# Kernel optimization log

Hardware: AMD Instinct MI355X
Metric: run time of the kernel (lower is better)

The kernel has to match this reference:

```python
import jax, jax.numpy as jnp
import numpy as np

THRESH = 0.001
RADIUS = 0.1
NSAMPLE = 8
FRAME_DIM = 6
LOSS_WEIGHT = 1.0
EPS = 1e-7


def _ball_query(new_xyz, xyz, radius, nsample):
    # new_xyz: [N,3] query points; xyz: [F,3] candidate points
    # pointnet2 semantics: first `nsample` in-radius indices (in order),
    # remaining slots filled with the first found index (0 if none).
    d2 = jnp.sum((new_xyz[:, None, :] - xyz[None, :, :]) ** 2, axis=-1)  # [N,F]
    mask = d2 < radius * radius
    order = jnp.argsort(~mask, axis=1)[:, :nsample]          # stable: in-radius idx first
    cnt = jnp.sum(mask, axis=1)                               # [N]
    valid = jnp.arange(nsample)[None, :] < cnt[:, None]       # [N,nsample]
    return jnp.where(valid, order, order[:, :1])              # [N,nsample] int


def _face_normals(verts, faces):
    # verts: [M,3], faces: [F,3] -> unit normals [F,3]
    v = verts[faces]                                           # [F,3,3]
    n = jnp.cross(v[:, 1] - v[:, 0], v[:, 2] - v[:, 0])        # [F,3]
    norm = jnp.linalg.norm(n, axis=-1, keepdims=True)
    return n / jnp.maximum(norm, EPS)


def _contact_error_single(pred, state, h_state, h_faces):
    x_t1 = pred[:, :3]                                         # [N,3]
    x_t0 = state[:, :3]                                        # [N,3]
    h_t1 = h_state[:, :3]                                      # [M,3]
    h_t0 = h_state[:, FRAME_DIM:FRAME_DIM + 3]                 # [M,3]
    h_face_pos = jnp.mean(h_t1[h_faces], axis=-2)              # [F,3]
    h_face_prev_pos = jnp.mean(h_t0[h_faces], axis=-2)         # [F,3]
    h_face_normal = _face_normals(h_t1, h_faces)               # [F,3]
    idx = _ball_query(x_t0, h_face_prev_pos, RADIUS, NSAMPLE)  # [N,S]
    grouped_pos = h_face_pos[idx]                              # [N,S,3]
    grouped_normal = h_face_normal[idx]                        # [N,S,3]
    xyz_diff = jnp.sum((x_t1[:, None, :] - grouped_pos) * grouped_normal,
                       axis=-1, keepdims=True)                 # [N,S,1]
    interpen = jnp.maximum(THRESH - xyz_diff, 0.0)
    loss = jnp.sum(interpen ** 3, axis=-2)                     # [N,1]
    return jnp.mean(loss)                                      # reduction='mean'


def setup_inputs() -> dict:
    key = jax.random.key(0)
    k1, k2, k3, k4 = jax.random.split(key, 4)
    B, N, M, F = 2, 20000, 6890, 13776
    pred = jax.random.normal(k1, (B, N, 3), dtype=jnp.float32)
    state = jax.random.normal(k2, (B, N, 3), dtype=jnp.float32)
    h_state = jax.random.normal(k3, (B, M, 9), dtype=jnp.float32)
    h_faces = jax.random.randint(k4, (B, F, 3), 0, M, dtype=jnp.int32)
    return {"pred": pred, "state": state, "h_state": h_state, "h_faces": h_faces}


def reference(pred, state, h_state, h_faces):
    per_sample = jax.vmap(_contact_error_single)(pred, state, h_state, h_faces)  # [B]
    return jnp.mean(per_sample) * LOSS_WEIGHT
```

## Files before the change

kernel.cpp:

```cpp
#include <hip/hip_runtime.h>
#include <limits.h>

#define NB      2
#define N_Q     20000
#define NBQ     (NB * N_Q)
#define M_V     6890
#define N_F     13776
#define NBF     (NB * N_F)
#define RAD2    0.01f
#define THRESH  0.001f
#define EPSN    1e-7f
#define SCALE   (1.0f / (float)(NB * N_Q))

#define GDIM    12
#define NCELLS  (GDIM * GDIM * GDIM)
#define T_CELLS (NB * NCELLS)
#define H_INV   5.0f
#define ORG     (-1.2f)

#define CAP     128

#define QPB     8
#define QBLOCKS (NBQ / QPB)

__device__ __forceinline__ int cell_coord(float x) {
    int g = (int)floorf((x - ORG) * H_INV);
    return min(max(g, 0), GDIM - 1);
}

__device__ __forceinline__ void axis_window(float v, int& lo, int& hi) {
    float s  = (v - ORG) * H_INV;
    float fl = floorf(s);
    int g_u  = (int)fl;
    int g    = min(max(g_u, 0), GDIM - 1);
    int sy   = ((s - fl) >= 0.5f) ? 1 : -1;
    int g2   = min(max(g_u + sy, 0), GDIM - 1);
    lo = min(g, g2);
    hi = max(g, g2);
}

__device__ __forceinline__ float wave_add_f(float v) {
    #pragma unroll
    for (int m = 32; m; m >>= 1) v += __shfl_xor(v, m);
    return v;
}
__device__ __forceinline__ int half_min_i(int v) {
    #pragma unroll
    for (int m = 16; m; m >>= 1) v = min(v, __shfl_xor(v, m));
    return v;
}

__global__ __launch_bounds__(256) void face_kernel(
    const float* __restrict__ h_state,
    const int*   __restrict__ h_faces,
    float4* __restrict__ posn,
    float4* __restrict__ buckets,
    int* __restrict__ cellCnt)
{
    int t = blockIdx.x * 256 + threadIdx.x;
    if (t >= NBF) return;
    int b = t / N_F;
    const int* fc = h_faces + (size_t)t * 3;
    int i0 = fc[0], i1 = fc[1], i2 = fc[2];
    const float* hs = h_state + (size_t)b * M_V * 9;

    const float* v0 = hs + (size_t)i0 * 9;
    const float* v1 = hs + (size_t)i1 * 9;
    const float* v2 = hs + (size_t)i2 * 9;

    float ax = v0[0], ay = v0[1], az = v0[2];
    float bx = v1[0], by = v1[1], bz = v1[2];
    float cx = v2[0], cy = v2[1], cz = v2[2];

    float px = (ax + bx + cx) / 3.0f;
    float py = (ay + by + cy) / 3.0f;
    float pz = (az + bz + cz) / 3.0f;

    float e1x = bx - ax, e1y = by - ay, e1z = bz - az;
    float e2x = cx - ax, e2y = cy - ay, e2z = cz - az;
    float nx = e1y * e2z - e1z * e2y;
    float ny = e1z * e2x - e1x * e2z;
    float nz = e1x * e2y - e1y * e2x;
    float nrm = sqrtf(nx * nx + ny * ny + nz * nz);
    float den = fmaxf(nrm, EPSN);
    nx /= den; ny /= den; nz /= den;

    float qx = (v0[6] + v1[6] + v2[6]) / 3.0f;
    float qy = (v0[7] + v1[7] + v2[7]) / 3.0f;
    float qz = (v0[8] + v1[8] + v2[8]) / 3.0f;

    posn[2 * t]     = make_float4(px, py, pz, 0.0f);
    posn[2 * t + 1] = make_float4(nx, ny, nz, 0.0f);

    int gx = cell_coord(qx), gy = cell_coord(qy), gz = cell_coord(qz);
    int cid = b * NCELLS + (gz * GDIM + gy) * GDIM + gx;
    int slot = atomicAdd(&cellCnt[cid], 1);
    if (slot < CAP)
        buckets[(size_t)cid * CAP + slot] = make_float4(qx, qy, qz, __int_as_float(t));
}

#define CSW(a, b) { int _mn = min(a, b); int _mx = max(a, b); a = _mn; b = _mx; }

__global__ __launch_bounds__(256) void query_kernel(
    const float*  __restrict__ state,
    const float*  __restrict__ pred,
    const float4* __restrict__ buckets,
    const float4* __restrict__ posn,
    const int* __restrict__ cellCnt,
    float* __restrict__ partials)
{
    __shared__ float ws[QPB];

    int tid  = threadIdx.x;
    int l32  = tid & 31;
    int hw   = tid >> 5;
    int q    = blockIdx.x * QPB + hw;
    int b    = (q >= N_Q) ? 1 : 0;

    const float* st = state + (size_t)q * 3;
    float qx = st[0], qy = st[1], qz = st[2];
    const float* pr = pred + (size_t)q * 3;
    float x = pr[0], y = pr[1], z = pr[2];

    float4 P0 = posn[2 * (b * N_F)];
    float4 N0 = posn[2 * (b * N_F) + 1];

    int xlo, xhi, ylo, yhi, zlo, zhi;
    axis_window(qx, xlo, xhi);
    axis_window(qy, ylo, yhi);
    axis_window(qz, zlo, zhi);

    int cum1, cum2, cum3, cum4, cum5, cum6, cum7, cum8;
    int off0, off1, off2, off3, off4, off5, off6, off7;
    {
        int bN = b * NCELLS;
        #define CELL(CI, CUMP, CUMN, OFFR)                                  \
        {                                                                   \
            int gz = zlo + ((CI) >> 2);                                     \
            int gy = ylo + (((CI) >> 1) & 1);                               \
            int gx = xlo + ((CI) & 1);                                      \
            int len = 0, base = 0;                                          \
            if (gz <= zhi && gy <= yhi && gx <= xhi) {                      \
                int c = bN + (gz * GDIM + gy) * GDIM + gx;                  \
                len = cellCnt[c];                                           \
                base = c * CAP;                                             \
            }                                                               \
            OFFR = base - CUMP;                                             \
            CUMN = CUMP + len;                                              \
        }
        int c0 = 0;
        CELL(0, c0,   cum1, off0)
        CELL(1, cum1, cum2, off1)
        CELL(2, cum2, cum3, off2)
        CELL(3, cum3, cum4, off3)
        CELL(4, cum4, cum5, off4)
        CELL(5, cum5, cum6, off5)
        CELL(6, cum6, cum7, off6)
        CELL(7, cum7, cum8, off7)
        #undef CELL
    }
    int C = cum8;

    int s0 = INT_MAX, s1 = INT_MAX, s2 = INT_MAX, s3 = INT_MAX;
    int s4 = INT_MAX, s5 = INT_MAX, s6 = INT_MAX, s7 = INT_MAX;
    int cnt = 0;
    float fsum = 0.0f;
    int   lmin = INT_MAX;
    float fmin = 0.0f;

    int iters = (C + 31) >> 5;
    for (int it = 0; it < iters; ++it) {
        int k = (it << 5) + l32;
        int addr = off0 + k;
        addr = (k >= cum1) ? off1 + k : addr;
        addr = (k >= cum2) ? off2 + k : addr;
        addr = (k >= cum3) ? off3 + k : addr;
        addr = (k >= cum4) ? off4 + k : addr;
        addr = (k >= cum5) ? off5 + k : addr;
        addr = (k >= cum6) ? off6 + k : addr;
        addr = (k >= cum7) ? off7 + k : addr;
        if (k < C) {
            float4 p = buckets[addr];
            float ddx = p.x - qx, ddy = p.y - qy, ddz = p.z - qz;
            float d2 = ddx * ddx + ddy * ddy + ddz * ddz;
            if (d2 < RAD2) {
                ++cnt;
                int tf = __float_as_int(p.w);
                float4 P  = posn[2 * tf];
                float4 Nn = posn[2 * tf + 1];
                float d = (x - P.x) * Nn.x + (y - P.y) * Nn.y + (z - P.z) * Nn.z;
                float ip = fmaxf(THRESH - d, 0.0f);
                float f = ip * ip * ip;
                fsum += f;
                if (tf < lmin) { lmin = tf; fmin = f; }
                if (tf < s7) {
                    s7 = tf;
                    CSW(s6, s7); CSW(s5, s6); CSW(s4, s5); CSW(s3, s4);
                    CSW(s2, s3); CSW(s1, s2); CSW(s0, s1);
                }
            }
        }
    }

    int   c_ = cnt;
    float fs = fsum;
    int   lm = lmin;
    float fm = fmin;
    #pragma unroll
    for (int m = 16; m; m >>= 1) {
        int   oc = __shfl_xor(c_, m);
        float os = __shfl_xor(fs, m);
        int   ol = __shfl_xor(lm, m);
        float of = __shfl_xor(fm, m);
        c_ += oc;
        fs += os;
        if (ol < lm) { lm = ol; fm = of; }
    }
    int cnt_tot = c_;

    float lsum;
    if (cnt_tot == 0) {
        float d0 = (x - P0.x) * N0.x + (y - P0.y) * N0.y + (z - P0.z) * N0.z;
        float ip0 = fmaxf(THRESH - d0, 0.0f);
        lsum = 8.0f * (ip0 * ip0 * ip0);
    } else if (cnt_tot <= 8) {
        lsum = fs + (float)(8 - cnt_tot) * fm;
    } else {
        int t0, t1, t2, t3, t4, t5, t6, t7;
#define EXTRACT(TK)                                                      \
        {                                                                \
            int m = half_min_i(s0);                                      \
            TK = m;                                                      \
            bool p = (s0 == m);                                          \
            s0 = p ? s1 : s0; s1 = p ? s2 : s1; s2 = p ? s3 : s2;        \
            s3 = p ? s4 : s3; s4 = p ? s5 : s4; s5 = p ? s6 : s5;        \
            s6 = p ? s7 : s6; s7 = p ? INT_MAX : s7;                     \
        }
        EXTRACT(t0) EXTRACT(t1) EXTRACT(t2) EXTRACT(t3)
        EXTRACT(t4) EXTRACT(t5) EXTRACT(t6) EXTRACT(t7)
#undef EXTRACT
        int v = t0;
        v = (l32 == 1) ? t1 : v;
        v = (l32 == 2) ? t2 : v;
        v = (l32 == 3) ? t3 : v;
        v = (l32 == 4) ? t4 : v;
        v = (l32 == 5) ? t5 : v;
        v = (l32 == 6) ? t6 : v;
        v = (l32 == 7) ? t7 : v;
        float4 P  = posn[2 * v];
        float4 Nn = posn[2 * v + 1];
        float d = (x - P.x) * Nn.x + (y - P.y) * Nn.y + (z - P.z) * Nn.z;
        float ip = fmaxf(THRESH - d, 0.0f);
        float c = ip * ip * ip;
        c = (l32 < 8) ? c : 0.0f;
        #pragma unroll
        for (int m = 16; m; m >>= 1) c += __shfl_xor(c, m);
        lsum = c;
    }

    if (l32 == 0) ws[hw] = lsum;
    __syncthreads();
    if (tid == 0) {
        float s = 0.0f;
        #pragma unroll
        for (int k = 0; k < QPB; ++k) s += ws[k];
        partials[blockIdx.x] = s;
    }
}

__global__ __launch_bounds__(1024) void reduce_kernel(
    const float* __restrict__ partials, float* __restrict__ out)
{
    float s = 0.0f;
    for (int i = threadIdx.x; i < QBLOCKS; i += 1024)
        s += partials[i];
    s = wave_add_f(s);
    __shared__ float ws[16];
    int lane = threadIdx.x & 63, w = threadIdx.x >> 6;
    if (lane == 0) ws[w] = s;
    __syncthreads();
    if (threadIdx.x == 0) {
        float t = 0.0f;
        #pragma unroll
        for (int i = 0; i < 16; ++i) t += ws[i];
        out[0] = t * SCALE;
    }
}

extern "C" void kernel_launch(void* const* d_in, const int* in_sizes, int n_in,
                              void* d_out, int out_size, void* d_ws, size_t ws_size,
                              hipStream_t stream) {
    const float* pred    = (const float*)d_in[0];
    const float* state   = (const float*)d_in[1];
    const float* h_state = (const float*)d_in[2];
    const int*   h_faces = (const int*)d_in[3];
    float* out = (float*)d_out;

    float4* posn    = (float4*)d_ws;
    float4* buckets = posn + 2 * NBF;
    int* cellCnt    = (int*)(buckets + (size_t)T_CELLS * CAP);
    float* partials = (float*)(cellCnt + T_CELLS);

    hipMemsetAsync(cellCnt, 0, (size_t)T_CELLS * sizeof(int), stream);

    face_kernel<<<dim3((NBF + 255) / 256), 256, 0, stream>>>(
        h_state, h_faces, posn, buckets, cellCnt);

    query_kernel<<<dim3(QBLOCKS), 256, 0, stream>>>(
        state, pred, buckets, posn, cellCnt, partials);

    reduce_kernel<<<dim3(1), 1024, 0, stream>>>(partials, out);
}
```

Before: 40.48 us.

## Assign 8 lanes per query instead of 32 and vectorize face vertex loads

The query kernel now maps each ball query to an 8-lane group instead of a 32-lane half-wave, so a block handles 32 queries. Shuffle reductions, the top-8 extraction and the block reduction are reworked to match. With few candidates per query, this is meant to cut idle lanes and reduce the number of blocks. The face kernel also reads vertex data with float4 loads, one covering x,y,z and one covering the prev position. Those loads assume 16-byte alignment at rows with a 36-byte stride, which is not guaranteed and risks misaligned access.

Result: slower. 42.53 us (+5.1%).

```diff
diff --git a/kernel.cpp b/kernel.cpp
--- a/kernel.cpp
+++ b/kernel.cpp
@@ -20,8 +20,9 @@
 
 #define CAP     128
 
-#define QPB     8
+#define QPB     32
 #define QBLOCKS (NBQ / QPB)
+#define B_SPLIT (N_Q / QPB)
 
 __device__ __forceinline__ int cell_coord(float x) {
     int g = (int)floorf((x - ORG) * H_INV);
@@ -44,9 +45,9 @@
     for (int m = 32; m; m >>= 1) v += __shfl_xor(v, m);
     return v;
 }
-__device__ __forceinline__ int half_min_i(int v) {
+__device__ __forceinline__ int group_min_i(int v) {
     #pragma unroll
-    for (int m = 16; m; m >>= 1) v = min(v, __shfl_xor(v, m));
+    for (int m = 4; m; m >>= 1) v = min(v, __shfl_xor(v, m));
     return v;
 }
 
@@ -67,17 +68,19 @@
     const float* v0 = hs + (size_t)i0 * 9;
     const float* v1 = hs + (size_t)i1 * 9;
     const float* v2 = hs + (size_t)i2 * 9;
-
-    float ax = v0[0], ay = v0[1], az = v0[2];
-    float bx = v1[0], by = v1[1], bz = v1[2];
-    float cx = v2[0], cy = v2[1], cz = v2[2];
-
-    float px = (ax + bx + cx) / 3.0f;
-    float py = (ay + by + cy) / 3.0f;
-    float pz = (az + bz + cz) / 3.0f;
-
-    float e1x = bx - ax, e1y = by - ay, e1z = bz - az;
-    float e2x = cx - ax, e2y = cy - ay, e2z = cz - az;
+    float4 a0 = *(const float4*)(v0);
+    float4 a1 = *(const float4*)(v0 + 5);
+    float4 b0 = *(const float4*)(v1);
+    float4 b1 = *(const float4*)(v1 + 5);
+    float4 c0 = *(const float4*)(v2);
+    float4 c1 = *(const float4*)(v2 + 5);
+
+    float px = (a0.x + b0.x + c0.x) / 3.0f;
+    float py = (a0.y + b0.y + c0.y) / 3.0f;
+    float pz = (a0.z + b0.z + c0.z) / 3.0f;
+
+    float e1x = b0.x - a0.x, e1y = b0.y - a0.y, e1z = b0.z - a0.z;
+    float e2x = c0.x - a0.x, e2y = c0.y - a0.y, e2z = c0.z - a0.z;
     float nx = e1y * e2z - e1z * e2y;
     float ny = e1z * e2x - e1x * e2z;
     float nz = e1x * e2y - e1y * e2x;
@@ -85,9 +88,9 @@
     float den = fmaxf(nrm, EPSN);
     nx /= den; ny /= den; nz /= den;
 
-    float qx = (v0[6] + v1[6] + v2[6]) / 3.0f;
-    float qy = (v0[7] + v1[7] + v2[7]) / 3.0f;
-    float qz = (v0[8] + v1[8] + v2[8]) / 3.0f;
+    float qx = (a1.y + b1.y + c1.y) / 3.0f;
+    float qy = (a1.z + b1.z + c1.z) / 3.0f;
+    float qz = (a1.w + b1.w + c1.w) / 3.0f;
 
     posn[2 * t]     = make_float4(px, py, pz, 0.0f);
     posn[2 * t + 1] = make_float4(nx, ny, nz, 0.0f);
@@ -109,13 +112,13 @@
     const int* __restrict__ cellCnt,
     float* __restrict__ partials)
 {
-    __shared__ float ws[QPB];
+    __shared__ float ws[4];
 
     int tid  = threadIdx.x;
-    int l32  = tid & 31;
-    int hw   = tid >> 5;
-    int q    = blockIdx.x * QPB + hw;
-    int b    = (q >= N_Q) ? 1 : 0;
+    int l8   = tid & 7;
+    int g    = tid >> 3;
+    int q    = blockIdx.x * QPB + g;
+    int b    = (blockIdx.x >= B_SPLIT) ? 1 : 0;
 
     const float* st = state + (size_t)q * 3;
     float qx = st[0], qy = st[1], qz = st[2];
@@ -168,9 +171,9 @@
     int   lmin = INT_MAX;
     float fmin = 0.0f;
 
-    int iters = (C + 31) >> 5;
+    int iters = (C + 7) >> 3;
     for (int it = 0; it < iters; ++it) {
-        int k = (it << 5) + l32;
+        int k = (it << 3) + l8;
         int addr = off0 + k;
         addr = (k >= cum1) ? off1 + k : addr;
         addr = (k >= cum2) ? off2 + k : addr;
@@ -207,7 +210,7 @@
     int   lm = lmin;
     float fm = fmin;
     #pragma unroll
-    for (int m = 16; m; m >>= 1) {
+    for (int m = 4; m; m >>= 1) {
         int   oc = __shfl_xor(c_, m);
         float os = __shfl_xor(fs, m);
         int   ol = __shfl_xor(lm, m);
@@ -229,7 +232,7 @@
         int t0, t1, t2, t3, t4, t5, t6, t7;
 #define EXTRACT(TK)                                                      \
         {                                                                \
-            int m = half_min_i(s0);                                      \
+            int m = group_min_i(s0);                                     \
             TK = m;                                                      \
             bool p = (s0 == m);                                          \
             s0 = p ? s1 : s0; s1 = p ? s2 : s1; s2 = p ? s3 : s2;        \
@@ -240,32 +243,31 @@
         EXTRACT(t4) EXTRACT(t5) EXTRACT(t6) EXTRACT(t7)
 #undef EXTRACT
         int v = t0;
-        v = (l32 == 1) ? t1 : v;
-        v = (l32 == 2) ? t2 : v;
-        v = (l32 == 3) ? t3 : v;
-        v = (l32 == 4) ? t4 : v;
-        v = (l32 == 5) ? t5 : v;
-        v = (l32 == 6) ? t6 : v;
-        v = (l32 == 7) ? t7 : v;
+        v = (l8 == 1) ? t1 : v;
+        v = (l8 == 2) ? t2 : v;
+        v = (l8 == 3) ? t3 : v;
+        v = (l8 == 4) ? t4 : v;
+        v = (l8 == 5) ? t5 : v;
+        v = (l8 == 6) ? t6 : v;
+        v = (l8 == 7) ? t7 : v;
         float4 P  = posn[2 * v];
         float4 Nn = posn[2 * v + 1];
         float d = (x - P.x) * Nn.x + (y - P.y) * Nn.y + (z - P.z) * Nn.z;
         float ip = fmaxf(THRESH - d, 0.0f);
         float c = ip * ip * ip;
-        c = (l32 < 8) ? c : 0.0f;
         #pragma unroll
-        for (int m = 16; m; m >>= 1) c += __shfl_xor(c, m);
+        for (int m = 4; m; m >>= 1) c += __shfl_xor(c, m);
         lsum = c;
     }
 
-    if (l32 == 0) ws[hw] = lsum;
+    float c = (l8 == 0) ? lsum : 0.0f;
+    c += __shfl_xor(c, 8);
+    c += __shfl_xor(c, 16);
+    c += __shfl_xor(c, 32);
+    if ((tid & 63) == 0) ws[tid >> 6] = c;
     __syncthreads();
-    if (tid == 0) {
-        float s = 0.0f;
-        #pragma unroll
-        for (int k = 0; k < QPB; ++k) s += ws[k];
-        partials[blockIdx.x] = s;
-    }
+    if (tid == 0)
+        partials[blockIdx.x] = ws[0] + ws[1] + ws[2] + ws[3];
 }
 
 __global__ __launch_bounds__(1024) void reduce_kernel(
```
